# Kernel tuning notes

Hardware: AMD Instinct MI355X
Metric: run time of the kernel (lower is better)

The kernel has to match this reference:

```python
import jax, jax.numpy as jnp
import numpy as np

HIDDEN = 896
N_HEADS = 14
N_KV_HEADS = 2
HEAD_DIM = HIDDEN // N_HEADS  # 64
KV_GROUPS = N_HEADS // N_KV_HEADS  # 7
ROPE_THETA = 1000000.0


def rotate_half(x):
    x1, x2 = x[..., : x.shape[-1] // 2], x[..., x.shape[-1] // 2 :]
    return jnp.concatenate((-x2, x1), axis=-1)


def rope_tables(seq_len, dtype=jnp.float32):
    inv_freq = 1.0 / (ROPE_THETA ** (jnp.arange(0, HEAD_DIM, 2, dtype=jnp.float32) / HEAD_DIM))
    t = jnp.arange(seq_len, dtype=jnp.float32)
    freqs = jnp.outer(t, inv_freq)            # [S, D/2]
    emb = jnp.concatenate((freqs, freqs), -1)  # [S, D]
    return jnp.cos(emb).astype(dtype), jnp.sin(emb).astype(dtype)


def setup_inputs() -> dict:
    key = jax.random.key(0)
    ks = jax.random.split(key, 8)
    B, S = 2, 2048
    s = 0.02
    return {
        "hidden_states": jax.random.normal(ks[0], (B, S, HIDDEN), jnp.float32),
        "wq": jax.random.normal(ks[1], (HIDDEN, N_HEADS * HEAD_DIM), jnp.float32) * s,
        "bq": jnp.zeros((N_HEADS * HEAD_DIM,), jnp.float32),
        "wk": jax.random.normal(ks[2], (HIDDEN, N_KV_HEADS * HEAD_DIM), jnp.float32) * s,
        "bk": jnp.zeros((N_KV_HEADS * HEAD_DIM,), jnp.float32),
        "wv": jax.random.normal(ks[3], (HIDDEN, N_KV_HEADS * HEAD_DIM), jnp.float32) * s,
        "bv": jnp.zeros((N_KV_HEADS * HEAD_DIM,), jnp.float32),
        "wo": jax.random.normal(ks[4], (N_HEADS * HEAD_DIM, HIDDEN), jnp.float32) * s,
    }


def reference(hidden_states, wq, bq, wk, bk, wv, bv, wo):
    B, S, _ = hidden_states.shape
    q = (hidden_states @ wq + bq).reshape(B, S, N_HEADS, HEAD_DIM)
    k = (hidden_states @ wk + bk).reshape(B, S, N_KV_HEADS, HEAD_DIM)
    v = (hidden_states @ wv + bv).reshape(B, S, N_KV_HEADS, HEAD_DIM)

    cos, sin = rope_tables(S, hidden_states.dtype)
    cos, sin = cos[None, :, None, :], sin[None, :, None, :]
    q = q * cos + rotate_half(q) * sin
    k = k * cos + rotate_half(k) * sin

    # GQA broadcast: repeat kv heads to match query heads
    k = jnp.repeat(k, KV_GROUPS, axis=2)
    v = jnp.repeat(v, KV_GROUPS, axis=2)

    # [B, H, S, S]
    scores = jnp.einsum("bqhd,bkhd->bhqk", q, k) / jnp.sqrt(jnp.asarray(HEAD_DIM, hidden_states.dtype))
    mask = jnp.tril(jnp.ones((S, S), dtype=jnp.bool_))
    scores = jnp.where(mask[None, None, :, :], scores, jnp.asarray(-1e9, scores.dtype))
    attn = jax.nn.softmax(scores, axis=-1)
    out = jnp.einsum("bhqk,bkhd->bqhd", attn, v).reshape(B, S, N_HEADS * HEAD_DIM)
    return out @ wo
```

## Files before the change

### kernel.cpp

```cpp
#include <hip/hip_runtime.h>

#define HID 896
#define NQ 896
#define NKV 128
#define NQKV 1152
#define NH 14
#define NKVH 2
#define GQ 7
#define DH 64
#define SEQ 2048
#define BATCH 2
#define TOK (BATCH*SEQ)

typedef __attribute__((ext_vector_type(8))) short short8;
typedef __attribute__((ext_vector_type(4))) float f32x4;
typedef __attribute__((ext_vector_type(4))) unsigned short us4;

__device__ __forceinline__ unsigned short f2bf(float x) {
  unsigned int u = __builtin_bit_cast(unsigned int, x);
  u = (u + 0x7fffu + ((u >> 16) & 1u)) >> 16;
  return (unsigned short)u;
}
__device__ __forceinline__ float bf2f(unsigned short b) {
  return __builtin_bit_cast(float, (unsigned int)b << 16);
}
__device__ __forceinline__ f32x4 fzero4() {
  f32x4 z; z[0]=0.f; z[1]=0.f; z[2]=0.f; z[3]=0.f; return z;
}
__device__ __forceinline__ unsigned int cvt_pk_bf16(float lo, float hi) {
  unsigned int r;
  asm("v_cvt_pk_bf16_f32 %0, %1, %2" : "=v"(r) : "v"(lo), "v"(hi));
  return r;
}
__device__ __forceinline__ void gload_lds16(const unsigned short* g, unsigned short* l) {
  __builtin_amdgcn_global_load_lds(
      (const __attribute__((address_space(1))) void*)(const void*)g,
      (__attribute__((address_space(3))) void*)(void*)l, 16, 0, 0);
}

#define CVT_BLKS 3584
#define TRN_BLKS 448
#define BIAS_BLKS 5
#define TAB_BLKS 256
#define PREP_BLKS (CVT_BLKS + TRN_BLKS + BIAS_BLKS + TAB_BLKS)

__global__ void k_prep(const float* __restrict__ hs,
                       const float* __restrict__ wq, const float* __restrict__ bq,
                       const float* __restrict__ wk, const float* __restrict__ bk,
                       const float* __restrict__ wv, const float* __restrict__ bv,
                       const float* __restrict__ wo,
                       unsigned short* __restrict__ hb,
                       unsigned short* __restrict__ wqkvt,
                       unsigned short* __restrict__ wot,
                       float* __restrict__ bqkv,
                       float2* __restrict__ cs) {
  __shared__ unsigned short Ls[64*65];
  int blk = blockIdx.x, tid = threadIdx.x;
  if (blk < CVT_BLKS) {
    int i = blk*256 + tid;
    float4 v = ((const float4*)hs)[i];
    us4 o; o[0]=f2bf(v.x); o[1]=f2bf(v.y); o[2]=f2bf(v.z); o[3]=f2bf(v.w);
    ((us4*)hb)[i] = o;
    return;
  }
  blk -= CVT_BLKS;
  if (blk < TRN_BLKS) {
    const float* W; unsigned short* out; int K, N, n0, k0;
    if (blk < 196)      { W=wq; out=wqkvt;                        K=HID; N=NQ;  int t=blk;     n0=(t%14)*64; k0=(t/14)*64; }
    else if (blk < 224) { W=wk; out=wqkvt + (size_t)NQ*HID;       K=HID; N=NKV; int t=blk-196; n0=(t%2)*64;  k0=(t/2)*64; }
    else if (blk < 252) { W=wv; out=wqkvt + (size_t)(NQ+NKV)*HID; K=HID; N=NKV; int t=blk-224; n0=(t%2)*64;  k0=(t/2)*64; }
    else                { W=wo; out=wot;                          K=NQ;  N=HID; int t=blk-252; n0=(t%14)*64; k0=(t/14)*64; }
    #pragma unroll
    for (int i = 0; i < 16; ++i) {
      int idx = i*256 + tid;
      int r = idx >> 6, c = idx & 63;
      Ls[c*65 + r] = f2bf(W[(size_t)(k0 + r)*N + n0 + c]);
    }
    __syncthreads();
    #pragma unroll
    for (int i = 0; i < 16; ++i) {
      int idx = i*256 + tid;
      int r2 = idx >> 6, c2 = idx & 63;
      out[(size_t)(n0 + r2)*K + k0 + c2] = Ls[r2*65 + c2];
    }
    return;
  }
  blk -= TRN_BLKS;
  if (blk < BIAS_BLKS) {
    int i = blk*256 + tid;
    if (i < NQKV) {
      if (i < NQ) bqkv[i] = bq[i];
      else if (i < NQ + NKV) bqkv[i] = bk[i - NQ];
      else bqkv[i] = bv[i - NQ - NKV];
    }
    return;
  }
  blk -= BIAS_BLKS;
  {
    int i = blk*256 + tid;
    int s = i >> 5, dp = i & 31;
    float inv = __expf(-(float)(2*dp) * (13.815510557964274f / 64.0f));
    float f = (float)s * inv;
    cs[i] = make_float2(cosf(f), sinf(f));
  }
}

template<int OUTMODE>
__global__ __launch_bounds__(256, 3) void k_gemm_bt(
    const unsigned short* __restrict__ A,
    const unsigned short* __restrict__ Bt,
    const float* __restrict__ bias,
    const float2* __restrict__ cs,
    void* __restrict__ Cout,
    unsigned short* __restrict__ Qr,
    unsigned short* __restrict__ Kr,
    unsigned short* __restrict__ Vt,
    int M, int N, int K) {
  __shared__ unsigned short As[2][64*64];
  __shared__ unsigned short Bs[2][128*64];
  int tid = threadIdx.x;
  int lane = tid & 63, w = tid >> 6;
  int wr = w >> 1, wc = w & 1;
  int l15 = lane & 15, l4 = lane >> 4;
  int m0 = blockIdx.y * 64, n0 = blockIdx.x * 128;

  f32x4 acc[2][4];
  #pragma unroll
  for (int i = 0; i < 2; ++i)
    #pragma unroll
    for (int j = 0; j < 4; ++j) acc[i][j] = fzero4();

  auto stage = [&](int kt, int bsel) {
    int k0 = kt << 6;
    #pragma unroll
    for (int t = 0; t < 2; ++t) {
      int chunk = t*256 + w*64 + lane;
      int row = chunk >> 3, sp = chunk & 7;
      int sl = sp ^ (row & 7);
      gload_lds16(A + (size_t)(m0+row)*K + k0 + sl*8, &As[bsel][(t*256 + w*64)*8]);
    }
    #pragma unroll
    for (int t = 0; t < 4; ++t) {
      int chunk = t*256 + w*64 + lane;
      int row = chunk >> 3, sp = chunk & 7;
      int sl = sp ^ (row & 7);
      gload_lds16(Bt + (size_t)(n0+row)*K + k0 + sl*8, &Bs[bsel][(t*256 + w*64)*8]);
    }
  };

  int nkt = K >> 6;
  stage(0, 0);
  __syncthreads();
  int cur = 0;
  for (int kt = 0; kt < nkt; ++kt) {
    if (kt + 1 < nkt) stage(kt + 1, cur ^ 1);
    #pragma unroll
    for (int s = 0; s < 2; ++s) {
      short8 af[2], bfr[4];
      #pragma unroll
      for (int mi = 0; mi < 2; ++mi) {
        int row = wr*32 + mi*16 + l15;
        int slot = (s*4 + l4) ^ (row & 7);
        af[mi] = *reinterpret_cast<const short8*>(&As[cur][row*64 + slot*8]);
      }
      #pragma unroll
      for (int ni = 0; ni < 4; ++ni) {
        int row = wc*64 + ni*16 + l15;
        int slot = (s*4 + l4) ^ (row & 7);
        bfr[ni] = *reinterpret_cast<const short8*>(&Bs[cur][row*64 + slot*8]);
      }
      #pragma unroll
      for (int mi = 0; mi < 2; ++mi)
        #pragma unroll
        for (int ni = 0; ni < 4; ++ni)
          acc[mi][ni] = __builtin_amdgcn_mfma_f32_16x16x32_bf16(af[mi], bfr[ni], acc[mi][ni], 0, 0, 0);
    }
    __syncthreads();
    cur ^= 1;
  }

  if (OUTMODE == 1) {
    #pragma unroll
    for (int mi = 0; mi < 2; ++mi)
      #pragma unroll
      for (int ni = 0; ni < 4; ++ni)
        #pragma unroll
        for (int r = 0; r < 4; ++r) {
          int row = m0 + wr*32 + mi*16 + l4*4 + r;
          int col = n0 + wc*64 + ni*16 + l15;
          ((float*)Cout)[(size_t)row*N + col] = acc[mi][ni][r];
        }
    return;
  }

  int col0 = n0 + wc*64;
  if (col0 < NQ + NKV) {
    #pragma unroll
    for (int mi = 0; mi < 2; ++mi) {
      #pragma unroll
      for (int r = 0; r < 4; ++r) {
        int row = m0 + wr*32 + mi*16 + l4*4 + r;
        int b = row >> 11, s = row & 2047;
        #pragma unroll
        for (int ni = 0; ni < 2; ++ni) {
          int dp = ni*16 + l15;
          float x1 = acc[mi][ni][r]   + bias[col0 + dp];
          float x2 = acc[mi][ni+2][r] + bias[col0 + dp + 32];
          float2 c2 = cs[s*32 + dp];
          if (col0 < NQ) {
            int h = col0 >> 6;
            size_t base = ((size_t)(b*NH + h)*SEQ + s)*64;
            Qr[base + dp]      = f2bf((x1*c2.x - x2*c2.y) * 0.125f);
            Qr[base + dp + 32] = f2bf((x2*c2.x + x1*c2.y) * 0.125f);
          } else {
            int kvh = (col0 - NQ) >> 6;
            size_t base = ((size_t)(b*NKVH + kvh)*SEQ + s)*64;
            Kr[base + dp]      = f2bf(x1*c2.x - x2*c2.y);
            Kr[base + dp + 32] = f2bf(x2*c2.x + x1*c2.y);
          }
        }
      }
    }
  } else {
    int kvh = (col0 - 1024) >> 6;
    unsigned short* scr = &Bs[0][0] + w * (64*40);
    #pragma unroll
    for (int mi = 0; mi < 2; ++mi) {
      #pragma unroll
      for (int ni = 0; ni < 2; ++ni) {
        #pragma unroll
        for (int h2 = 0; h2 < 2; ++h2) {
          int dp = ni*16 + l15 + h2*32;
          float b0 = bias[col0 + dp];
          f32x4 a = acc[mi][ni + h2*2];
          uint2 pk;
          pk.x = cvt_pk_bf16(a[0] + b0, a[1] + b0);
          pk.y = cvt_pk_bf16(a[2] + b0, a[3] + b0);
          *reinterpret_cast<uint2*>(&scr[dp*40 + mi*16 + l4*4]) = pk;
        }
      }
    }
    __syncthreads();
    int srow0 = m0 + wr*32;
    int b = srow0 >> 11, s0 = srow0 & 2047;
    size_t vbase = (size_t)(b*NKVH + kvh)*64;
    #pragma unroll
    for (int p2 = 0; p2 < 4; ++p2) {
      int dp = p2*16 + (lane >> 2);
      int tok0 = (lane & 3) * 8;
      short8 v = *reinterpret_cast<const short8*>(&scr[dp*40 + tok0]);
      *reinterpret_cast<short8*>(&Vt[(vbase + dp)*SEQ + s0 + tok0]) = v;
    }
  }
}

__global__ __launch_bounds__(512, 2) void k_attn(
    const unsigned short* __restrict__ Q,
    const unsigned short* __restrict__ Kr,
    const unsigned short* __restrict__ Vt,
    unsigned short* __restrict__ Aout) {
  __shared__ __align__(16) unsigned short Kst[2][64*64];
  __shared__ __align__(16) unsigned short Vst[2][64*64];
  __shared__ __align__(16) unsigned short P_lds[8][16*64];
  int lane = threadIdx.x & 63, w = threadIdx.x >> 6;
  int grp = w >> 2, wsub = w & 3;
  int l15 = lane & 15, l4 = lane >> 4;
  int sb = (int)gridDim.x - 1 - (int)blockIdx.x;
  int h = blockIdx.y, b = blockIdx.z;
  int qt = 2*sb + grp;
  int kvh = h / GQ;
  const unsigned short* Kb = Kr + ((size_t)(b*NKVH + kvh))*SEQ*64;
  const unsigned short* Vb = Vt + ((size_t)(b*NKVH + kvh))*64*SEQ;
  char* Pw = (char*)&P_lds[w][0];

  auto stage = [&](int ks, int bsel) {
    int chunk = w*64 + lane;
    int row = chunk >> 3;
    int sl = (chunk & 7) ^ (row & 7);
    gload_lds16(Kb + (size_t)(ks*64 + row)*64 + sl*8, &Kst[bsel][chunk*8]);
    gload_lds16(Vb + (size_t)row*SEQ + ks*64 + sl*8, &Vst[bsel][chunk*8]);
  };

  const unsigned short* Qb = Q + (((size_t)(b*NH + h))*SEQ + qt*64 + wsub*16) * 64;
  short8 qa[2];
  #pragma unroll
  for (int s = 0; s < 2; ++s)
    qa[s] = *reinterpret_cast<const short8*>(Qb + l15*64 + s*32 + l4*8);

  f32x4 acc[4];
  #pragma unroll
  for (int n = 0; n < 4; ++n) acc[n] = fzero4();
  float m_run = -__builtin_inff(), l_run = 0.0f;

  stage(0, 0);
  __syncthreads();
  int cur = 0;
  int nkt = 2*sb + 2;

  for (int kt = 0; kt < nkt; ++kt) {
    if (kt + 1 < nkt) stage(kt + 1, cur ^ 1);
    if (kt <= qt) {
      const unsigned short* Ks = &Kst[cur][0];
      const unsigned short* Vs = &Vst[cur][0];
      f32x4 sa[4];
      #pragma unroll
      for (int n = 0; n < 4; ++n) sa[n] = fzero4();
      __builtin_amdgcn_s_setprio(1);
      #pragma unroll
      for (int si = 0; si < 2; ++si) {
        short8 kb[4];
        #pragma unroll
        for (int n = 0; n < 4; ++n) {
          int row = n*16 + l15;
          int slot = (si*4 + l4) ^ (row & 7);
          kb[n] = *reinterpret_cast<const short8*>(&Ks[row*64 + slot*8]);
        }
        #pragma unroll
        for (int n = 0; n < 4; ++n)
          sa[n] = __builtin_amdgcn_mfma_f32_16x16x32_bf16(kb[n], qa[si], sa[n], 0, 0, 0);
      }
      __builtin_amdgcn_s_setprio(0);
      if (kt == qt) {
        int q_glob = qt*64 + wsub*16 + l15;
        #pragma unroll
        for (int n = 0; n < 4; ++n)
          #pragma unroll
          for (int r = 0; r < 4; ++r) {
            int kpos = kt*64 + n*16 + l4*4 + r;
            if (kpos > q_glob) sa[n][r] = -1e30f;
          }
      }
      float t0 = fmaxf(fmaxf(sa[0][0],sa[0][1]), fmaxf(sa[0][2],sa[0][3]));
      float t1 = fmaxf(fmaxf(sa[1][0],sa[1][1]), fmaxf(sa[1][2],sa[1][3]));
      float t2 = fmaxf(fmaxf(sa[2][0],sa[2][1]), fmaxf(sa[2][2],sa[2][3]));
      float t3 = fmaxf(fmaxf(sa[3][0],sa[3][1]), fmaxf(sa[3][2],sa[3][3]));
      float tmax = fmaxf(fmaxf(t0,t1), fmaxf(t2,t3));
      tmax = fmaxf(tmax, __shfl_xor(tmax, 16));
      tmax = fmaxf(tmax, __shfl_xor(tmax, 32));
      float mn = fmaxf(m_run, tmax);
      float sc = __expf(m_run - mn);
      #pragma unroll
      for (int n = 0; n < 4; ++n)
        #pragma unroll
        for (int r = 0; r < 4; ++r) sa[n][r] = __expf(sa[n][r] - mn);
      float s0 = (sa[0][0]+sa[0][1]) + (sa[0][2]+sa[0][3]);
      float s1 = (sa[1][0]+sa[1][1]) + (sa[1][2]+sa[1][3]);
      float s2 = (sa[2][0]+sa[2][1]) + (sa[2][2]+sa[2][3]);
      float s3 = (sa[3][0]+sa[3][1]) + (sa[3][2]+sa[3][3]);
      float sum = (s0+s1) + (s2+s3);
      m_run = mn;
      l_run = l_run*sc + sum;
      #pragma unroll
      for (int n = 0; n < 4; ++n) acc[n] *= sc;
      #pragma unroll
      for (int n = 0; n < 4; ++n) {
        uint2 pk;
        pk.x = cvt_pk_bf16(sa[n][0], sa[n][1]);
        pk.y = cvt_pk_bf16(sa[n][2], sa[n][3]);
        int colbyte = n*32 + l4*8;
        int addr = l15*128 + ((((colbyte>>4) ^ (l15&7))) << 4) + (colbyte & 15);
        *reinterpret_cast<uint2*>(Pw + addr) = pk;
      }
      __builtin_amdgcn_s_setprio(1);
      #pragma unroll
      for (int s2i = 0; s2i < 2; ++s2i) {
        int pslot = (s2i*4 + l4) ^ (l15 & 7);
        short8 pa = *reinterpret_cast<const short8*>(Pw + l15*128 + pslot*16);
        #pragma unroll
        for (int n = 0; n < 4; ++n) {
          int row = n*16 + l15;
          int vslot = (s2i*4 + l4) ^ (row & 7);
          short8 vb = *reinterpret_cast<const short8*>(&Vs[row*64 + vslot*8]);
          acc[n] = __builtin_amdgcn_mfma_f32_16x16x32_bf16(vb, pa, acc[n], 0, 0, 0);
        }
      }
      __builtin_amdgcn_s_setprio(0);
    }
    __syncthreads();
    cur ^= 1;
  }

  float lt = l_run;
  lt += __shfl_xor(lt, 16);
  lt += __shfl_xor(lt, 32);
  float inv = 1.0f / lt;
  #pragma unroll
  for (int n = 0; n < 4; ++n) {
    uint2 pk;
    pk.x = cvt_pk_bf16(acc[n][0]*inv, acc[n][1]*inv);
    pk.y = cvt_pk_bf16(acc[n][2]*inv, acc[n][3]*inv);
    int colbyte = n*32 + l4*8;
    int addr = l15*128 + ((((colbyte>>4) ^ (l15&7))) << 4) + (colbyte & 15);
    *reinterpret_cast<uint2*>(Pw + addr) = pk;
  }
  int row = lane >> 2;
  int cb0 = (lane & 3) * 32;
  #pragma unroll
  for (int it = 0; it < 2; ++it) {
    int cb = cb0 + it*16;
    int slot = (cb >> 4) ^ (row & 7);
    short8 v = *reinterpret_cast<const short8*>(Pw + row*128 + slot*16);
    size_t tok = (size_t)b*SEQ + qt*64 + wsub*16 + row;
    *reinterpret_cast<short8*>(&Aout[tok*NQ + h*64 + (cb>>1)]) = v;
  }
}

extern "C" void kernel_launch(void* const* d_in, const int* in_sizes, int n_in,
                              void* d_out, int out_size, void* d_ws, size_t ws_size,
                              hipStream_t stream) {
  const float* hs = (const float*)d_in[0];
  const float* wq = (const float*)d_in[1];
  const float* bq = (const float*)d_in[2];
  const float* wk = (const float*)d_in[3];
  const float* bk = (const float*)d_in[4];
  const float* wv = (const float*)d_in[5];
  const float* bv = (const float*)d_in[6];
  const float* wo = (const float*)d_in[7];
  float* out = (float*)d_out;

  char* p = (char*)d_ws;
  auto alloc = [&](size_t bytes) { char* r = p; p += (bytes + 255) & ~(size_t)255; return r; };
  unsigned short* hb    = (unsigned short*)alloc((size_t)TOK*HID*2);
  unsigned short* wqkvt = (unsigned short*)alloc((size_t)NQKV*HID*2);
  unsigned short* wot   = (unsigned short*)alloc((size_t)HID*NQ*2);
  float*          bqkv  = (float*)alloc(NQKV*4);
  float2*         cs    = (float2*)alloc((size_t)SEQ*32*8);
  unsigned short* q_r   = (unsigned short*)alloc((size_t)BATCH*NH*SEQ*DH*2);
  unsigned short* k_r   = (unsigned short*)alloc((size_t)BATCH*NKVH*SEQ*DH*2);
  unsigned short* v_t   = (unsigned short*)alloc((size_t)BATCH*NKVH*DH*SEQ*2);
  unsigned short* attn  = (unsigned short*)alloc((size_t)TOK*NQ*2);

  k_prep<<<PREP_BLKS, 256, 0, stream>>>(hs, wq, bq, wk, bk, wv, bv, wo,
                                        hb, wqkvt, wot, bqkv, cs);
  k_gemm_bt<0><<<dim3(NQKV/128, TOK/64), 256, 0, stream>>>(
      hb, wqkvt, bqkv, cs, nullptr, q_r, k_r, v_t, TOK, NQKV, HID);
  k_attn<<<dim3(16, NH, BATCH), 512, 0, stream>>>(q_r, k_r, v_t, attn);
  k_gemm_bt<1><<<dim3(NQ/128, TOK/64), 256, 0, stream>>>(
      attn, wot, nullptr, nullptr, out, nullptr, nullptr, nullptr, TOK, NQ, HID);
}
```

Before: 103.2 us.

## Give each attention wave 32 query rows and pair complementary causal tiles per block

The attention kernel now uses 256-thread blocks of 4 waves, and each wave handles 32 query rows (two 16-row subtiles). Each K/V fragment read from LDS therefore feeds twice as many MFMAs. Each block also pairs query tile i with tile 31-i, so every block does about the same causal work, replacing the previous pairing of adjacent tiles. The cost is more accumulator registers per wave, which the launch bounds of 3 blocks per CU may constrain, and fewer waves in flight per block to hide latency.

```diff
diff --git a/kernel.cpp b/kernel.cpp
--- a/kernel.cpp
+++ b/kernel.cpp
@@ -254,57 +254,67 @@
   }
 }
 
-__global__ __launch_bounds__(512, 2) void k_attn(
+__global__ __launch_bounds__(256, 3) void k_attn(
     const unsigned short* __restrict__ Q,
     const unsigned short* __restrict__ Kr,
     const unsigned short* __restrict__ Vt,
     unsigned short* __restrict__ Aout) {
   __shared__ __align__(16) unsigned short Kst[2][64*64];
   __shared__ __align__(16) unsigned short Vst[2][64*64];
-  __shared__ __align__(16) unsigned short P_lds[8][16*64];
+  __shared__ __align__(16) unsigned short P_lds[4][32*64];
   int lane = threadIdx.x & 63, w = threadIdx.x >> 6;
-  int grp = w >> 2, wsub = w & 3;
+  int grp = w >> 1, wsub = w & 1;
   int l15 = lane & 15, l4 = lane >> 4;
-  int sb = (int)gridDim.x - 1 - (int)blockIdx.x;
-  int h = blockIdx.y, b = blockIdx.z;
-  int qt = 2*sb + grp;
+  int i = blockIdx.x, h = blockIdx.y, b = blockIdx.z;
+  int qtH = 31 - i, qtL = i;
+  int qt = grp ? qtL : qtH;
   int kvh = h / GQ;
   const unsigned short* Kb = Kr + ((size_t)(b*NKVH + kvh))*SEQ*64;
   const unsigned short* Vb = Vt + ((size_t)(b*NKVH + kvh))*64*SEQ;
   char* Pw = (char*)&P_lds[w][0];
 
   auto stage = [&](int ks, int bsel) {
-    int chunk = w*64 + lane;
-    int row = chunk >> 3;
-    int sl = (chunk & 7) ^ (row & 7);
-    gload_lds16(Kb + (size_t)(ks*64 + row)*64 + sl*8, &Kst[bsel][chunk*8]);
-    gload_lds16(Vb + (size_t)row*SEQ + ks*64 + sl*8, &Vst[bsel][chunk*8]);
+    #pragma unroll
+    for (int part = 0; part < 2; ++part) {
+      int chunk = part*256 + threadIdx.x;
+      int row = chunk >> 3;
+      int sl = (chunk & 7) ^ (row & 7);
+      gload_lds16(Kb + (size_t)(ks*64 + row)*64 + sl*8, &Kst[bsel][chunk*8]);
+      gload_lds16(Vb + (size_t)row*SEQ + ks*64 + sl*8, &Vst[bsel][chunk*8]);
+    }
   };
 
-  const unsigned short* Qb = Q + (((size_t)(b*NH + h))*SEQ + qt*64 + wsub*16) * 64;
-  short8 qa[2];
+  const unsigned short* Qb = Q + (((size_t)(b*NH + h))*SEQ + qt*64 + wsub*32) * 64;
+  short8 qa[2][2];
   #pragma unroll
-  for (int s = 0; s < 2; ++s)
-    qa[s] = *reinterpret_cast<const short8*>(Qb + l15*64 + s*32 + l4*8);
-
-  f32x4 acc[4];
+  for (int st = 0; st < 2; ++st)
+    #pragma unroll
+    for (int si = 0; si < 2; ++si)
+      qa[st][si] = *reinterpret_cast<const short8*>(Qb + (size_t)(st*16 + l15)*64 + si*32 + l4*8);
+
+  f32x4 acc[2][4];
   #pragma unroll
-  for (int n = 0; n < 4; ++n) acc[n] = fzero4();
-  float m_run = -__builtin_inff(), l_run = 0.0f;
+  for (int st = 0; st < 2; ++st)
+    #pragma unroll
+    for (int n = 0; n < 4; ++n) acc[st][n] = fzero4();
+  float m_run[2] = { -__builtin_inff(), -__builtin_inff() };
+  float l_run[2] = { 0.0f, 0.0f };
 
   stage(0, 0);
   __syncthreads();
   int cur = 0;
-  int nkt = 2*sb + 2;
+  int nkt = qtH + 1;
 
   for (int kt = 0; kt < nkt; ++kt) {
     if (kt + 1 < nkt) stage(kt + 1, cur ^ 1);
     if (kt <= qt) {
       const unsigned short* Ks = &Kst[cur][0];
       const unsigned short* Vs = &Vst[cur][0];
-      f32x4 sa[4];
-      #pragma unroll
-      for (int n = 0; n < 4; ++n) sa[n] = fzero4();
+      f32x4 sa[2][4];
+      #pragma unroll
+      for (int st = 0; st < 2; ++st)
+        #pragma unroll
+        for (int n = 0; n < 4; ++n) sa[st][n] = fzero4();
       __builtin_amdgcn_s_setprio(1);
       #pragma unroll
       for (int si = 0; si < 2; ++si) {
@@ -316,62 +326,76 @@
           kb[n] = *reinterpret_cast<const short8*>(&Ks[row*64 + slot*8]);
         }
         #pragma unroll
-        for (int n = 0; n < 4; ++n)
-          sa[n] = __builtin_amdgcn_mfma_f32_16x16x32_bf16(kb[n], qa[si], sa[n], 0, 0, 0);
+        for (int st = 0; st < 2; ++st)
+          #pragma unroll
+          for (int n = 0; n < 4; ++n)
+            sa[st][n] = __builtin_amdgcn_mfma_f32_16x16x32_bf16(kb[n], qa[st][si], sa[st][n], 0, 0, 0);
       }
       __builtin_amdgcn_s_setprio(0);
       if (kt == qt) {
-        int q_glob = qt*64 + wsub*16 + l15;
+        #pragma unroll
+        for (int st = 0; st < 2; ++st) {
+          int q_glob = qt*64 + wsub*32 + st*16 + l15;
+          #pragma unroll
+          for (int n = 0; n < 4; ++n)
+            #pragma unroll
+            for (int r = 0; r < 4; ++r) {
+              int kpos = kt*64 + n*16 + l4*4 + r;
+              if (kpos > q_glob) sa[st][n][r] = -1e30f;
+            }
+        }
+      }
+      #pragma unroll
+      for (int st = 0; st < 2; ++st) {
+        float t0 = fmaxf(fmaxf(sa[st][0][0],sa[st][0][1]), fmaxf(sa[st][0][2],sa[st][0][3]));
+        float t1 = fmaxf(fmaxf(sa[st][1][0],sa[st][1][1]), fmaxf(sa[st][1][2],sa[st][1][3]));
+        float t2 = fmaxf(fmaxf(sa[st][2][0],sa[st][2][1]), fmaxf(sa[st][2][2],sa[st][2][3]));
+        float t3 = fmaxf(fmaxf(sa[st][3][0],sa[st][3][1]), fmaxf(sa[st][3][2],sa[st][3][3]));
+        float tmax = fmaxf(fmaxf(t0,t1), fmaxf(t2,t3));
+        tmax = fmaxf(tmax, __shfl_xor(tmax, 16));
+        tmax = fmaxf(tmax, __shfl_xor(tmax, 32));
+        float mn = fmaxf(m_run[st], tmax);
+        float sc = __expf(m_run[st] - mn);
         #pragma unroll
         for (int n = 0; n < 4; ++n)
           #pragma unroll
-          for (int r = 0; r < 4; ++r) {
-            int kpos = kt*64 + n*16 + l4*4 + r;
-            if (kpos > q_glob) sa[n][r] = -1e30f;
-          }
-      }
-      float t0 = fmaxf(fmaxf(sa[0][0],sa[0][1]), fmaxf(sa[0][2],sa[0][3]));
-      float t1 = fmaxf(fmaxf(sa[1][0],sa[1][1]), fmaxf(sa[1][2],sa[1][3]));
-      float t2 = fmaxf(fmaxf(sa[2][0],sa[2][1]), fmaxf(sa[2][2],sa[2][3]));
-      float t3 = fmaxf(fmaxf(sa[3][0],sa[3][1]), fmaxf(sa[3][2],sa[3][3]));
-      float tmax = fmaxf(fmaxf(t0,t1), fmaxf(t2,t3));
-      tmax = fmaxf(tmax, __shfl_xor(tmax, 16));
-      tmax = fmaxf(tmax, __shfl_xor(tmax, 32));
-      float mn = fmaxf(m_run, tmax);
-      float sc = __expf(m_run - mn);
-      #pragma unroll
-      for (int n = 0; n < 4; ++n)
-        #pragma unroll
-        for (int r = 0; r < 4; ++r) sa[n][r] = __expf(sa[n][r] - mn);
-      float s0 = (sa[0][0]+sa[0][1]) + (sa[0][2]+sa[0][3]);
-      float s1 = (sa[1][0]+sa[1][1]) + (sa[1][2]+sa[1][3]);
-      float s2 = (sa[2][0]+sa[2][1]) + (sa[2][2]+sa[2][3]);
-      float s3 = (sa[3][0]+sa[3][1]) + (sa[3][2]+sa[3][3]);
-      float sum = (s0+s1) + (s2+s3);
-      m_run = mn;
-      l_run = l_run*sc + sum;
-      #pragma unroll
-      for (int n = 0; n < 4; ++n) acc[n] *= sc;
-      #pragma unroll
-      for (int n = 0; n < 4; ++n) {
-        uint2 pk;
-        pk.x = cvt_pk_bf16(sa[n][0], sa[n][1]);
-        pk.y = cvt_pk_bf16(sa[n][2], sa[n][3]);
-        int colbyte = n*32 + l4*8;
-        int addr = l15*128 + ((((colbyte>>4) ^ (l15&7))) << 4) + (colbyte & 15);
-        *reinterpret_cast<uint2*>(Pw + addr) = pk;
+          for (int r = 0; r < 4; ++r) sa[st][n][r] = __expf(sa[st][n][r] - mn);
+        float s0 = (sa[st][0][0]+sa[st][0][1]) + (sa[st][0][2]+sa[st][0][3]);
+        float s1 = (sa[st][1][0]+sa[st][1][1]) + (sa[st][1][2]+sa[st][1][3]);
+        float s2 = (sa[st][2][0]+sa[st][2][1]) + (sa[st][2][2]+sa[st][2][3]);
+        float s3 = (sa[st][3][0]+sa[st][3][1]) + (sa[st][3][2]+sa[st][3][3]);
+        float sum = (s0+s1) + (s2+s3);
+        m_run[st] = mn;
+        l_run[st] = l_run[st]*sc + sum;
+        #pragma unroll
+        for (int n = 0; n < 4; ++n) acc[st][n] *= sc;
+        #pragma unroll
+        for (int n = 0; n < 4; ++n) {
+          uint2 pk;
+          pk.x = cvt_pk_bf16(sa[st][n][0], sa[st][n][1]);
+          pk.y = cvt_pk_bf16(sa[st][n][2], sa[st][n][3]);
+          int colbyte = n*32 + l4*8;
+          int row = st*16 + l15;
+          int addr = row*128 + ((((colbyte>>4) ^ (l15&7))) << 4) + (colbyte & 15);
+          *reinterpret_cast<uint2*>(Pw + addr) = pk;
+        }
       }
       __builtin_amdgcn_s_setprio(1);
       #pragma unroll
       for (int s2i = 0; s2i < 2; ++s2i) {
         int pslot = (s2i*4 + l4) ^ (l15 & 7);
-        short8 pa = *reinterpret_cast<const short8*>(Pw + l15*128 + pslot*16);
+        short8 pa[2];
+        #pragma unroll
+        for (int st = 0; st < 2; ++st)
+          pa[st] = *reinterpret_cast<const short8*>(Pw + (st*16 + l15)*128 + pslot*16);
         #pragma unroll
         for (int n = 0; n < 4; ++n) {
           int row = n*16 + l15;
           int vslot = (s2i*4 + l4) ^ (row & 7);
           short8 vb = *reinterpret_cast<const short8*>(&Vs[row*64 + vslot*8]);
-          acc[n] = __builtin_amdgcn_mfma_f32_16x16x32_bf16(vb, pa, acc[n], 0, 0, 0);
+          #pragma unroll
+          for (int st = 0; st < 2; ++st)
+            acc[st][n] = __builtin_amdgcn_mfma_f32_16x16x32_bf16(vb, pa[st], acc[st][n], 0, 0, 0);
         }
       }
       __builtin_amdgcn_s_setprio(0);
@@ -380,28 +404,32 @@
     cur ^= 1;
   }
 
-  float lt = l_run;
-  lt += __shfl_xor(lt, 16);
-  lt += __shfl_xor(lt, 32);
-  float inv = 1.0f / lt;
   #pragma unroll
-  for (int n = 0; n < 4; ++n) {
-    uint2 pk;
-    pk.x = cvt_pk_bf16(acc[n][0]*inv, acc[n][1]*inv);
-    pk.y = cvt_pk_bf16(acc[n][2]*inv, acc[n][3]*inv);
-    int colbyte = n*32 + l4*8;
-    int addr = l15*128 + ((((colbyte>>4) ^ (l15&7))) << 4) + (colbyte & 15);
-    *reinterpret_cast<uint2*>(Pw + addr) = pk;
-  }
-  int row = lane >> 2;
-  int cb0 = (lane & 3) * 32;
-  #pragma unroll
-  for (int it = 0; it < 2; ++it) {
-    int cb = cb0 + it*16;
-    int slot = (cb >> 4) ^ (row & 7);
-    short8 v = *reinterpret_cast<const short8*>(Pw + row*128 + slot*16);
-    size_t tok = (size_t)b*SEQ + qt*64 + wsub*16 + row;
-    *reinterpret_cast<short8*>(&Aout[tok*NQ + h*64 + (cb>>1)]) = v;
+  for (int st = 0; st < 2; ++st) {
+    float lt = l_run[st];
+    lt += __shfl_xor(lt, 16);
+    lt += __shfl_xor(lt, 32);
+    float inv = 1.0f / lt;
+    #pragma unroll
+    for (int n = 0; n < 4; ++n) {
+      uint2 pk;
+      pk.x = cvt_pk_bf16(acc[st][n][0]*inv, acc[st][n][1]*inv);
+      pk.y = cvt_pk_bf16(acc[st][n][2]*inv, acc[st][n][3]*inv);
+      int colbyte = n*32 + l4*8;
+      int row = st*16 + l15;
+      int addr = row*128 + ((((colbyte>>4) ^ (l15&7))) << 4) + (colbyte & 15);
+      *reinterpret_cast<uint2*>(Pw + addr) = pk;
+    }
+    int row16 = lane >> 2;
+    int cb0 = (lane & 3) * 32;
+    #pragma unroll
+    for (int it = 0; it < 2; ++it) {
+      int cb = cb0 + it*16;
+      int slot = (cb >> 4) ^ (row16 & 7);
+      short8 v = *reinterpret_cast<const short8*>(Pw + (st*16 + row16)*128 + slot*16);
+      size_t tok = (size_t)b*SEQ + qt*64 + wsub*32 + st*16 + row16;
+      *reinterpret_cast<short8*>(&Aout[tok*NQ + h*64 + (cb>>1)]) = v;
+    }
   }
 }
 
@@ -434,7 +462,7 @@
                                         hb, wqkvt, wot, bqkv, cs);
   k_gemm_bt<0><<<dim3(NQKV/128, TOK/64), 256, 0, stream>>>(
       hb, wqkvt, bqkv, cs, nullptr, q_r, k_r, v_t, TOK, NQKV, HID);
-  k_attn<<<dim3(16, NH, BATCH), 512, 0, stream>>>(q_r, k_r, v_t, attn);
+  k_attn<<<dim3(16, NH, BATCH), 256, 0, stream>>>(q_r, k_r, v_t, attn);
   k_gemm_bt<1><<<dim3(NQ/128, TOK/64), 256, 0, stream>>>(
       attn, wot, nullptr, nullptr, out, nullptr, nullptr, nullptr, TOK, NQ, HID);
 }
```

Result: slower. 107.1 us (+3.7%).
